# Optimization experiments

Measured on AMD Instinct MI355X. Metric: run time of the kernel, lower is better.

## Reference

```python
import jax, jax.numpy as jnp
import numpy as np

B = 524288
IN_DIM = 16
OUT_DIM = 32  # hidden_dim3
N_CHUNKS = 4
CHUNK = 4


def ste_round(x):
    # straight-through round (grad passes unchanged, like Round.apply)
    return x + jax.lax.stop_gradient(jnp.round(x) - x)


def ste_sign(x):
    # straight-through sign (grad passes unchanged, like Sign.apply)
    return x + jax.lax.stop_gradient(jnp.sign(x) - x)


def setup_inputs() -> dict:
    key = jax.random.key(0)
    k1, k2 = jax.random.split(key)
    Input = jax.random.uniform(k1, (B, IN_DIM), dtype=jnp.float32)
    weight = jax.random.normal(k2, (OUT_DIM, IN_DIM), dtype=jnp.float32)
    InMin = jnp.float32(0.0)
    InMax = jnp.float32(1.0)
    return {"Input": Input, "weight": weight, "InMin": InMin, "InMax": InMax}


def reference(Input, weight, InMin, InMax):
    # eval-mode forward of QuantLinear
    scale = InMax - InMin
    w = ste_sign(weight)                       # [O, I] in {-1, 0, 1}
    wP = jax.nn.relu(w)                        # positive mask
    wM = jax.nn.relu(-w)                       # negative mask

    # 4-bit input quantization (eval path): clip(round((x-min)/(max-min)*15), 0, 15)
    q = jnp.clip(ste_round((Input - InMin) / scale * 15.0), 0.0, 15.0)  # [B, I]

    # bias = linear(InMin * ones, w): each row = InMin * sum_j w[o, j]
    bias = InMin * jnp.sum(w, axis=1)          # [O], broadcasts over batch

    # chunked 4-wide linears, vectorized over the 4 chunks
    qc = q.reshape(B, N_CHUNKS, CHUNK)         # [B, C, 4]
    wPc = wP.reshape(OUT_DIM, N_CHUNKS, CHUNK)  # [O, C, 4]
    wMc = wM.reshape(OUT_DIM, N_CHUNKS, CHUNK)
    yP = jnp.einsum('bcf,ocf->cbo', qc, wPc)   # [C, B, O]
    yM = jnp.einsum('bcf,ocf->cbo', qc, wMc)   # [C, B, O]

    # accumulate clip(round(y/15), -4, 4) * (InMax - InMin) over all 8 terms
    terms = jnp.clip(ste_round(yP / 15.0), -4.0, 4.0) \
          + jnp.clip(ste_round(-yM / 15.0), -4.0, 4.0)  # [C, B, O]
    x = jnp.sum(terms, axis=0) * scale + bias  # [B, O]
    return x
```

## Files before the change

### kernel.cpp

```cpp
#include <hip/hip_runtime.h>
#include <stdint.h>


#if __has_builtin(__builtin_amdgcn_sdot4)
#define HAVE_SDOT4 1
#else
#define HAVE_SDOT4 0
#endif

__device__ __forceinline__ int dot7(uint32_t q, uint32_t m) {
#if HAVE_SDOT4
    return __builtin_amdgcn_sdot4((int)q, (int)m, 7, false);
#else
    return (int)(((q & m) * 0x01010101u) >> 24) + 7;
#endif
}

__device__ __forceinline__ int r15(int y7) {
    return (int)(((uint32_t)y7 * 274u) >> 12);
}

__global__ __launch_bounds__(256) void qlin_kernel(
    const float* __restrict__ in, const float* __restrict__ wgt,
    const float* __restrict__ pmin, const float* __restrict__ pmax,
    float* __restrict__ out, int nrows)
{
    __shared__ uint4 smask[64];
    __shared__ float sbias[32];

    const int t = threadIdx.x;
    const float InMin = pmin[0];
    const float InMax = pmax[0];
    const float scale = __fsub_rn(InMax, InMin);

    const uint32_t MASKBYTE = HAVE_SDOT4 ? 1u : 0xFFu;

    {
        int o = t >> 3, k = t & 7, c = k & 3, isM = k >> 2;
        const float* wrow = wgt + o * 16 + c * 4;
        uint32_t m = 0;
#pragma unroll
        for (int j = 0; j < 4; ++j) {
            float v = wrow[j];
            bool sel = isM ? (v < 0.0f) : (v > 0.0f);
            if (sel) m |= MASKBYTE << (8 * j);
        }
        ((uint32_t*)smask)[o * 8 + isM * 4 + c] = m;
    }
    __syncthreads();
    if (t < 32) {
        const uint32_t* mo = (const uint32_t*)smask + t * 8;
        int s = 0;
#pragma unroll
        for (int c = 0; c < 4; ++c)
            s += __popc(mo[c]) - __popc(mo[4 + c]);
        if (!HAVE_SDOT4) s /= 8;
        sbias[t] = __fmul_rn(InMin, (float)s);
    }
    __syncthreads();

    const int r = blockIdx.x * 256 + t;
    if (r >= nrows) return;

    const float4* inrow = (const float4*)in + (size_t)r * 4;
    const bool unit = (scale == 1.0f);
    uint32_t qp[4];
#pragma unroll
    for (int c = 0; c < 4; ++c) {
        float4 f = inrow[c];
        float e[4] = { f.x, f.y, f.z, f.w };
        uint32_t pk = 0;
#pragma unroll
        for (int j = 0; j < 4; ++j) {
            float d  = __fsub_rn(e[j], InMin);
            float sd = unit ? d : __fdiv_rn(d, scale);
            float v  = __fmul_rn(sd, 15.0f);
            float rr = rintf(v);
            rr = fminf(fmaxf(rr, 0.0f), 15.0f);
            pk |= ((uint32_t)(int)rr) << (8 * j);
        }
        qp[c] = pk;
    }

    float* orow = out + (size_t)r * 32;
#pragma unroll 2
    for (int og = 0; og < 8; ++og) {
        float res[4];
#pragma unroll
        for (int i = 0; i < 4; ++i) {
            int o = og * 4 + i;
            uint4 MP = smask[o * 2 + 0];
            uint4 MM = smask[o * 2 + 1];
            int acc = 0;
            acc += r15(dot7(qp[0], MP.x)) - r15(dot7(qp[0], MM.x));
            acc += r15(dot7(qp[1], MP.y)) - r15(dot7(qp[1], MM.y));
            acc += r15(dot7(qp[2], MP.z)) - r15(dot7(qp[2], MM.z));
            acc += r15(dot7(qp[3], MP.w)) - r15(dot7(qp[3], MM.w));
            res[i] = __fadd_rn(__fmul_rn((float)acc, scale), sbias[o]);
        }
        *(float4*)(orow + og * 4) = make_float4(res[0], res[1], res[2], res[3]);
    }
}

extern "C" void kernel_launch(void* const* d_in, const int* in_sizes, int n_in,
                              void* d_out, int out_size, void* d_ws, size_t ws_size,
                              hipStream_t stream) {
    (void)n_in; (void)d_ws; (void)ws_size; (void)out_size;
    const float* in  = (const float*)d_in[0];
    const float* wgt = (const float*)d_in[1];
    const float* mn  = (const float*)d_in[2];
    const float* mx  = (const float*)d_in[3];
    float* out = (float*)d_out;
    const int nrows = in_sizes[0] / 16;
    const int blocks = (nrows + 255) / 256;
    qlin_kernel<<<blocks, 256, 0, stream>>>(in, wgt, mn, mx, out, nrows);
}
```

Measured before the change: 111.8 us.

## Restructure to wave-cooperative rows with coalesced loads and stores plus grid-stride loop

Each wavefront now handles 16 rows per iteration. Every lane loads one float4 of input, so loads are fully coalesced, and the quantized words are spread to the lanes that need them with shuffles. Each lane keeps the masks for its 4 output columns in registers and writes one float4 for each of two rows, which makes the output stores contiguous across lanes. The launch becomes a fixed grid of 2048 blocks with a grid-stride loop and an occupancy hint. The new layout assumes nrows is a multiple of 16 (no tail handling) and adds shuffle overhead.

```diff
diff --git a/kernel.cpp b/kernel.cpp
--- a/kernel.cpp
+++ b/kernel.cpp
@@ -20,13 +20,13 @@
     return (int)(((uint32_t)y7 * 274u) >> 12);
 }
 
-__global__ __launch_bounds__(256) void qlin_kernel(
+__global__ __launch_bounds__(256, 6) void qlin_kernel(
     const float* __restrict__ in, const float* __restrict__ wgt,
     const float* __restrict__ pmin, const float* __restrict__ pmax,
     float* __restrict__ out, int nrows)
 {
     __shared__ uint4 smask[64];
-    __shared__ float sbias[32];
+    __shared__ __align__(16) float sbias[32];
 
     const int t = threadIdx.x;
     const float InMin = pmin[0];
@@ -59,17 +59,26 @@
     }
     __syncthreads();
 
-    const int r = blockIdx.x * 256 + t;
-    if (r >= nrows) return;
+    const int lane = t & 63;
+    const int ogrp = lane & 7;
+    const int rsel = lane >> 3;
+    const int srcb = rsel << 2;
 
-    const float4* inrow = (const float4*)in + (size_t)r * 4;
+    const uint4 MP0 = smask[(ogrp * 4 + 0) * 2], MM0 = smask[(ogrp * 4 + 0) * 2 + 1];
+    const uint4 MP1 = smask[(ogrp * 4 + 1) * 2], MM1 = smask[(ogrp * 4 + 1) * 2 + 1];
+    const uint4 MP2 = smask[(ogrp * 4 + 2) * 2], MM2 = smask[(ogrp * 4 + 2) * 2 + 1];
+    const uint4 MP3 = smask[(ogrp * 4 + 3) * 2], MM3 = smask[(ogrp * 4 + 3) * 2 + 1];
+    const float4 bias = *(const float4*)(sbias + ogrp * 4);
+
     const bool unit = (scale == 1.0f);
-    uint32_t qp[4];
-#pragma unroll
-    for (int c = 0; c < 4; ++c) {
-        float4 f = inrow[c];
+    const int gw = blockIdx.x * (256 >> 6) + (t >> 6);
+    const int nw = gridDim.x * (256 >> 6);
+
+    for (int R = gw * 16; R < nrows; R += nw * 16) {
+        const float4 f = *((const float4*)in + (size_t)R * 4 + lane);
+
         float e[4] = { f.x, f.y, f.z, f.w };
-        uint32_t pk = 0;
+        uint32_t qw = 0;
 #pragma unroll
         for (int j = 0; j < 4; ++j) {
             float d  = __fsub_rn(e[j], InMin);
@@ -77,28 +86,49 @@
             float v  = __fmul_rn(sd, 15.0f);
             float rr = rintf(v);
             rr = fminf(fmaxf(rr, 0.0f), 15.0f);
-            pk |= ((uint32_t)(int)rr) << (8 * j);
+            qw |= ((uint32_t)(int)rr) << (8 * j);
         }
-        qp[c] = pk;
-    }
 
-    float* orow = out + (size_t)r * 32;
-#pragma unroll 2
-    for (int og = 0; og < 8; ++og) {
-        float res[4];
-#pragma unroll
-        for (int i = 0; i < 4; ++i) {
-            int o = og * 4 + i;
-            uint4 MP = smask[o * 2 + 0];
-            uint4 MM = smask[o * 2 + 1];
-            int acc = 0;
-            acc += r15(dot7(qp[0], MP.x)) - r15(dot7(qp[0], MM.x));
-            acc += r15(dot7(qp[1], MP.y)) - r15(dot7(qp[1], MM.y));
-            acc += r15(dot7(qp[2], MP.z)) - r15(dot7(qp[2], MM.z));
-            acc += r15(dot7(qp[3], MP.w)) - r15(dot7(qp[3], MM.w));
-            res[i] = __fadd_rn(__fmul_rn((float)acc, scale), sbias[o]);
+        const uint32_t qA0 = __shfl(qw, srcb + 0, 64);
+        const uint32_t qA1 = __shfl(qw, srcb + 1, 64);
+        const uint32_t qA2 = __shfl(qw, srcb + 2, 64);
+        const uint32_t qA3 = __shfl(qw, srcb + 3, 64);
+        const uint32_t qB0 = __shfl(qw, 32 + srcb + 0, 64);
+        const uint32_t qB1 = __shfl(qw, 32 + srcb + 1, 64);
+        const uint32_t qB2 = __shfl(qw, 32 + srcb + 2, 64);
+        const uint32_t qB3 = __shfl(qw, 32 + srcb + 3, 64);
+
+        float* p0 = out + (size_t)(R + rsel) * 32 + (ogrp << 2);
+
+#define ROWCOMP(q0, q1, q2, q3, dst)                                        \
+        {                                                                   \
+            int a0 = r15(dot7(q0, MP0.x)) - r15(dot7(q0, MM0.x))            \
+                   + r15(dot7(q1, MP0.y)) - r15(dot7(q1, MM0.y))            \
+                   + r15(dot7(q2, MP0.z)) - r15(dot7(q2, MM0.z))            \
+                   + r15(dot7(q3, MP0.w)) - r15(dot7(q3, MM0.w));           \
+            int a1 = r15(dot7(q0, MP1.x)) - r15(dot7(q0, MM1.x))            \
+                   + r15(dot7(q1, MP1.y)) - r15(dot7(q1, MM1.y))            \
+                   + r15(dot7(q2, MP1.z)) - r15(dot7(q2, MM1.z))            \
+                   + r15(dot7(q3, MP1.w)) - r15(dot7(q3, MM1.w));           \
+            int a2 = r15(dot7(q0, MP2.x)) - r15(dot7(q0, MM2.x))            \
+                   + r15(dot7(q1, MP2.y)) - r15(dot7(q1, MM2.y))            \
+                   + r15(dot7(q2, MP2.z)) - r15(dot7(q2, MM2.z))            \
+                   + r15(dot7(q3, MP2.w)) - r15(dot7(q3, MM2.w));           \
+            int a3 = r15(dot7(q0, MP3.x)) - r15(dot7(q0, MM3.x))            \
+                   + r15(dot7(q1, MP3.y)) - r15(dot7(q1, MM3.y))            \
+                   + r15(dot7(q2, MP3.z)) - r15(dot7(q2, MM3.z))            \
+                   + r15(dot7(q3, MP3.w)) - r15(dot7(q3, MM3.w));           \
+            float4 res;                                                     \
+            res.x = __fadd_rn(__fmul_rn((float)a0, scale), bias.x);         \
+            res.y = __fadd_rn(__fmul_rn((float)a1, scale), bias.y);         \
+            res.z = __fadd_rn(__fmul_rn((float)a2, scale), bias.z);         \
+            res.w = __fadd_rn(__fmul_rn((float)a3, scale), bias.w);         \
+            *(float4*)(dst) = res;                                          \
         }
-        *(float4*)(orow + og * 4) = make_float4(res[0], res[1], res[2], res[3]);
+
+        ROWCOMP(qA0, qA1, qA2, qA3, p0);
+        ROWCOMP(qB0, qB1, qB2, qB3, p0 + 8 * 32);
+#undef ROWCOMP
     }
 }
 
@@ -112,6 +142,6 @@
     const float* mx  = (const float*)d_in[3];
     float* out = (float*)d_out;
     const int nrows = in_sizes[0] / 16;
-    const int blocks = (nrows + 255) / 256;
+    const int blocks = 2048;
     qlin_kernel<<<blocks, 256, 0, stream>>>(in, wgt, mn, mx, out, nrows);
 }
```

Measured after the change: 107.5 us. 1.04x faster.
